# Optimization experiments

Measured on AMD Instinct MI355X. Metric: run time of the kernel, lower is better.

The kernel has to match this reference:

```python
import jax, jax.numpy as jnp
import numpy as np

PATCH = 16
EPS = 1e-5


def _conv_offsets(x, offset_w, offset_b):
    # offset conv: same kernel/stride/padding as the deform conv
    off = jax.lax.conv_general_dilated(
        x, offset_w, window_strides=(PATCH, PATCH), padding='VALID',
        dimension_numbers=('NCHW', 'OIHW', 'NCHW'))
    return off + offset_b[None, :, None, None]


def _deform_conv(x, offset_w, offset_b, dconv_w):
    B, C, H, W = x.shape
    kh = kw = PATCH
    K = kh * kw
    Ho, Wo = H // PATCH, W // PATCH

    off = _conv_offsets(x, offset_w, offset_b)            # [B, 2K, Ho, Wo]
    # mmcv layout: channels are (dy, dx) pairs per kernel point
    off = off.reshape(B, K, 2, Ho, Wo)
    dy = off[:, :, 0].transpose(0, 2, 3, 1)               # [B, Ho, Wo, K]
    dx = off[:, :, 1].transpose(0, 2, 3, 1)

    ii, jj = jnp.meshgrid(jnp.arange(kh), jnp.arange(kw), indexing='ij')
    ki = ii.reshape(-1).astype(x.dtype)                   # [K]
    kj = jj.reshape(-1).astype(x.dtype)
    base_y = (jnp.arange(Ho, dtype=x.dtype) * PATCH)[:, None] + ki[None, :]  # [Ho, K]
    base_x = (jnp.arange(Wo, dtype=x.dtype) * PATCH)[:, None] + kj[None, :]  # [Wo, K]

    py = base_y[None, :, None, :] + dy                    # [B, Ho, Wo, K]
    px = base_x[None, None, :, :] + dx

    y0 = jnp.floor(py); x0 = jnp.floor(px)
    wy1 = py - y0; wx1 = px - x0
    wy0 = 1.0 - wy1; wx0 = 1.0 - wx1
    y0i = y0.astype(jnp.int32); x0i = x0.astype(jnp.int32)
    y1i = y0i + 1;              x1i = x0i + 1

    xt = x.transpose(0, 2, 3, 1)                          # [B, H, W, C]
    bidx = jnp.arange(B)[:, None, None, None]

    def gather(yi, xi):
        ok = ((yi >= 0) & (yi < H) & (xi >= 0) & (xi < W)).astype(x.dtype)
        v = xt[bidx, jnp.clip(yi, 0, H - 1), jnp.clip(xi, 0, W - 1)]  # [B,Ho,Wo,K,C]
        return v * ok[..., None]

    sampled = (gather(y0i, x0i) * (wy0 * wx0)[..., None]
               + gather(y0i, x1i) * (wy0 * wx1)[..., None]
               + gather(y1i, x0i) * (wy1 * wx0)[..., None]
               + gather(y1i, x1i) * (wy1 * wx1)[..., None])  # [B,Ho,Wo,K,C]

    Wk = dconv_w.reshape(dconv_w.shape[0], C, K)          # [O, C, K]
    out = jnp.einsum('bhwkc,ock->bohw', sampled, Wk)      # [B, O, Ho, Wo]
    return out


def setup_inputs() -> dict:
    key = jax.random.key(0)
    ks = jax.random.split(key, 3)
    B, C, H, W = 64, 3, 224, 224
    O = 768
    x = jax.random.normal(ks[0], (B, C, H, W), jnp.float32)
    # small offset weights -> offsets of O(1) pixel, exercising bilinear path
    offset_w = jax.random.normal(ks[1], (2 * PATCH * PATCH, C, PATCH, PATCH), jnp.float32) * 0.01
    offset_b = jnp.zeros((2 * PATCH * PATCH,), jnp.float32)
    dconv_w = jax.random.normal(ks[2], (O, C, PATCH, PATCH), jnp.float32) * 0.02
    bn_gamma = jnp.ones((O,), jnp.float32)
    bn_beta = jnp.zeros((O,), jnp.float32)
    return {"x": x, "offset_w": offset_w, "offset_b": offset_b,
            "dconv_w": dconv_w, "bn_gamma": bn_gamma, "bn_beta": bn_beta}


def reference(x, offset_w, offset_b, dconv_w, bn_gamma, bn_beta):
    B = x.shape[0]
    y = _deform_conv(x, offset_w, offset_b, dconv_w)      # [B, O, Ho, Wo]
    # BatchNorm2d (training-mode batch stats, biased var) per torch semantics
    mean = jnp.mean(y, axis=(0, 2, 3), keepdims=True)
    var = jnp.mean((y - mean) ** 2, axis=(0, 2, 3), keepdims=True)
    yn = (y - mean) * jax.lax.rsqrt(var + EPS)
    yn = yn * bn_gamma[None, :, None, None] + bn_beta[None, :, None, None]
    ya = jax.nn.gelu(yn, approximate=False)               # nn.GELU default = exact
    O, Ho, Wo = ya.shape[1], ya.shape[2], ya.shape[3]
    return ya.reshape(B, O, Ho * Wo).transpose(0, 2, 1)   # [B, N, embed_dim]
```

## Files before the change

### kernel.cpp

```cpp
#include <hip/hip_runtime.h>
#include <math.h>

#define PATCH 16
#define BATCH 64
#define CIN 3
#define HH 224
#define WW 224
#define NPATCH (BATCH*14*14)
#define KDIM 768
#define NOFF 512
#define NOUT 768
#define KPTS 256
#define EPSF 1e-5f
#define CHW (CIN*HH*WW)
#define HWX (HH*WW)
#define NRB (NPATCH/128)

using short8 = __attribute__((ext_vector_type(8))) short;
using f32x4  = __attribute__((ext_vector_type(4))) float;

#define GLOAD16(g, l) __builtin_amdgcn_global_load_lds( \
    (const __attribute__((address_space(1))) void*)(g), \
    (__attribute__((address_space(3))) void*)(l), 16, 0, 0)

__device__ __forceinline__ unsigned short f2bf(float f) {
    unsigned int u = __float_as_uint(f);
    u = (u + 0x7fffu + ((u >> 16) & 1u)) >> 16;
    return (unsigned short)u;
}
__device__ __forceinline__ float bf2f(unsigned short h) {
    return __uint_as_float(((unsigned int)h) << 16);
}
__device__ __forceinline__ float gelu_exact(float v) {
    return 0.5f * v * (1.0f + erff(v * 0.70710678118654752440f));
}

#define N4X (BATCH*CHW/4)
#define N4W1 (NOFF*KDIM/4)
#define N4W2 (NOUT*KDIM/4)
#define N4ALL (N4X+N4W1+N4W2)

__global__ __launch_bounds__(256) void cvt_all(
    const float* __restrict__ x, const float* __restrict__ w1,
    const float* __restrict__ w2, unsigned short* __restrict__ xbf,
    unsigned short* __restrict__ wbf1, unsigned short* __restrict__ wbf2)
{
    for (int i = blockIdx.x*256 + threadIdx.x; i < N4ALL; i += gridDim.x*256) {
        const float* src; unsigned short* dst; int j;
        if (i < N4X)            { src = x;  dst = xbf;  j = i; }
        else if (i < N4X+N4W1)  { src = w1; dst = wbf1; j = i - N4X; }
        else                    { src = w2; dst = wbf2; j = i - N4X - N4W1; }
        float4 v = ((const float4*)src)[j];
        ((ushort4*)dst)[j] = make_ushort4(f2bf(v.x), f2bf(v.y), f2bf(v.z), f2bf(v.w));
    }
}

__global__ __launch_bounds__(256) void gemm_offsets(
    const unsigned short* __restrict__ xbf, const unsigned short* __restrict__ Bw,
    const float* __restrict__ offb, unsigned short* __restrict__ off)
{
    __shared__ unsigned short lds[4*8192];
    const int t = threadIdx.x;
    const int lane = t & 63;
    const int w = t >> 6, wr = w >> 1, wc = w & 1;

    int bid = blockIdx.x;
    int idx = (bid & 7)*49 + (bid >> 3);
    const int bm = (idx >> 2) * 128, bn = (idx & 3) * 128;

    const int rq = t >> 2;
    const int ksw = (((t & 3) ^ ((t >> 3) & 3)) << 3);

    const unsigned short* aBase0;
    const unsigned short* aBase1;
    {
        int p0 = bm + rq,      b0 = p0/196, r0 = p0%196;
        int p1 = bm + 64 + rq, b1 = p1/196, r1 = p1%196;
        aBase0 = xbf + (size_t)b0*CHW + (size_t)((r0/14)*PATCH)*WW + (size_t)((r0%14)*PATCH);
        aBase1 = xbf + (size_t)b1*CHW + (size_t)((r1/14)*PATCH)*WW + (size_t)((r1%14)*PATCH);
    }
    const unsigned short* bS0 = Bw + (size_t)(bn + rq)*KDIM + ksw;
    const unsigned short* bS1 = Bw + (size_t)(bn + 64 + rq)*KDIM + ksw;

    const int row_a = wr*64 + (lane & 15);
    const int row_b = wc*64 + (lane & 15);
    const int klocs = (((lane >> 4) ^ ((lane >> 1) & 3)) << 3);

#define STG1(slot, k0) do { \
        unsigned short* d = lds + (slot)*8192 + t*8; \
        int e = (k0) + ksw; \
        size_t xo = (size_t)(e >> 8)*HWX + (size_t)((e >> 4) & 15)*WW + (e & 15); \
        GLOAD16(aBase0 + xo, d); \
        GLOAD16(aBase1 + xo, d + 2048); \
        GLOAD16(bS0 + (k0), d + 4096); \
        GLOAD16(bS1 + (k0), d + 6144); \
    } while(0)

    f32x4 acc[4][4] = {};
    STG1(0, 0); STG1(1, 32); STG1(2, 64);
    asm volatile("s_waitcnt vmcnt(8)" ::: "memory");
    __builtin_amdgcn_s_barrier();
#pragma unroll
    for (int it = 0; it < 24; ++it) {
        if (it + 3 < 24) STG1((it+3)&3, (it+3)*32);
        const unsigned short* As_ = lds + (it&3)*8192;
        const unsigned short* Bs_ = As_ + 4096;
        short8 af[4], bv[4];
#pragma unroll
        for (int m = 0; m < 4; ++m) af[m] = *(const short8*)&As_[(row_a + m*16)*32 + klocs];
#pragma unroll
        for (int n = 0; n < 4; ++n) bv[n] = *(const short8*)&Bs_[(row_b + n*16)*32 + klocs];
        __builtin_amdgcn_s_setprio(1);
#pragma unroll
        for (int m = 0; m < 4; ++m)
#pragma unroll
            for (int n = 0; n < 4; ++n)
                acc[m][n] = __builtin_amdgcn_mfma_f32_16x16x32_bf16(af[m], bv[n], acc[m][n], 0, 0, 0);
        __builtin_amdgcn_s_setprio(0);
        if (it <= 20)      { asm volatile("s_waitcnt vmcnt(8) lgkmcnt(0)" ::: "memory"); __builtin_amdgcn_s_barrier(); }
        else if (it == 21) { asm volatile("s_waitcnt vmcnt(4) lgkmcnt(0)" ::: "memory"); __builtin_amdgcn_s_barrier(); }
        else if (it == 22) { asm volatile("s_waitcnt vmcnt(0) lgkmcnt(0)" ::: "memory"); __builtin_amdgcn_s_barrier(); }
    }
#undef STG1

    const int col0 = bn + wc*64 + (lane & 15);
    const int r0 = (lane >> 4) * 4;
#pragma unroll
    for (int m = 0; m < 4; ++m) {
        int grow = bm + wr*64 + m*16 + r0;
#pragma unroll
        for (int n = 0; n < 4; ++n) {
            int gcol = col0 + n*16;
            float bias = offb[gcol];
#pragma unroll
            for (int r = 0; r < 4; ++r)
                off[(size_t)(grow + r)*NOFF + gcol] = f2bf(acc[m][n][r] + bias);
        }
    }
}

__global__ __launch_bounds__(256) void sampler(
    const unsigned short* __restrict__ xbf, const unsigned int* __restrict__ offu,
    unsigned short* __restrict__ A2)
{
    __shared__ unsigned short win[3][22][24];
    int p = blockIdx.x;
    int k = threadIdx.x;
    int b = p / 196, rem = p % 196;
    int ho = rem / 14, wo = rem % 14;
    const int gy0 = ho*PATCH - 2, gx0 = wo*PATCH - 2;
    const unsigned short* xb = xbf + (size_t)b*CHW;

    bool interior = (ho >= 1) && (ho <= 12) && (wo >= 1) && (wo <= 12);
    if (interior) {
        for (int idx = k; idx < 3*22*11; idx += 256) {
            int c = idx / 242, r2 = idx - c*242;
            int row = r2 / 11, u = r2 - row*11;
            const unsigned int* src = (const unsigned int*)
                (xb + (size_t)c*HWX + (size_t)(gy0+row)*WW + gx0);
            *(unsigned int*)&win[c][row][2*u] = src[u];
        }
    } else {
        for (int idx = k; idx < 3*22*22; idx += 256) {
            int c = idx / 484, r2 = idx - c*484;
            int row = r2 / 22, col = r2 - row*22;
            int gy = min(max(gy0+row, 0), HH-1);
            int gx = min(max(gx0+col, 0), WW-1);
            win[c][row][col] = xb[(size_t)c*HWX + (size_t)gy*WW + gx];
        }
    }
    __syncthreads();

    unsigned int d2 = offu[(size_t)p*KPTS + k];
    float dy = __uint_as_float((d2 & 0xffffu) << 16);
    float dx = __uint_as_float(d2 & 0xffff0000u);
    float py = (float)(ho*PATCH + (k >> 4)) + dy;
    float px = (float)(wo*PATCH + (k & 15)) + dx;
    float fy = floorf(py), fx = floorf(px);
    float wy1 = py - fy, wx1 = px - fx;
    float wy0 = 1.f - wy1, wx0 = 1.f - wx1;
    int y0 = (int)fy, x0 = (int)fx;
    int y1 = y0 + 1, x1 = x0 + 1;
    bool oky0 = (y0 >= 0) & (y0 < HH);
    bool oky1 = (y1 >= 0) & (y1 < HH);
    bool okx0 = (x0 >= 0) & (x0 < WW);
    bool okx1 = (x1 >= 0) & (x1 < WW);
    float w00 = wy0*wx0, w01 = wy0*wx1, w10 = wy1*wx0, w11 = wy1*wx1;

    int ry = y0 - gy0, rx = x0 - gx0;
    if (ry >= 0 && ry <= 20 && rx >= 0 && rx <= 20) {
        float m00 = oky0 && okx0 ? 1.f : 0.f;
        float m01 = oky0 && okx1 ? 1.f : 0.f;
        float m10 = oky1 && okx0 ? 1.f : 0.f;
        float m11 = oky1 && okx1 ? 1.f : 0.f;
#pragma unroll
        for (int c = 0; c < CIN; ++c) {
            float v00 = bf2f(win[c][ry  ][rx  ]) * m00;
            float v01 = bf2f(win[c][ry  ][rx+1]) * m01;
            float v10 = bf2f(win[c][ry+1][rx  ]) * m10;
            float v11 = bf2f(win[c][ry+1][rx+1]) * m11;
            float v = v00*w00 + v01*w01 + v10*w10 + v11*w11;
            A2[(size_t)p*KDIM + c*KPTS + k] = f2bf(v);
        }
    } else {
        int yc0 = min(max(y0, 0), HH-1), yc1 = min(max(y1, 0), HH-1);
        int xc0 = min(max(x0, 0), WW-1), xc1 = min(max(x1, 0), WW-1);
#pragma unroll
        for (int c = 0; c < CIN; ++c) {
            const unsigned short* xc = xb + (size_t)c*HWX;
            float v00 = (oky0 && okx0) ? bf2f(xc[(size_t)yc0*WW + xc0]) : 0.f;
            float v01 = (oky0 && okx1) ? bf2f(xc[(size_t)yc0*WW + xc1]) : 0.f;
            float v10 = (oky1 && okx0) ? bf2f(xc[(size_t)yc1*WW + xc0]) : 0.f;
            float v11 = (oky1 && okx1) ? bf2f(xc[(size_t)yc1*WW + xc1]) : 0.f;
            float v = v00*w00 + v01*w01 + v10*w10 + v11*w11;
            A2[(size_t)p*KDIM + c*KPTS + k] = f2bf(v);
        }
    }
}

__global__ __launch_bounds__(512) void gemm_deform(
    const unsigned short* __restrict__ A, const unsigned short* __restrict__ Bw,
    unsigned short* __restrict__ Cbf, float* __restrict__ psum, float* __restrict__ psq)
{
    __shared__ unsigned short lds[4*16384];
    const int t = threadIdx.x;
    const int lane = t & 63;
    const int w = t >> 6;
    const int wr = w >> 2, wc = w & 3;

    int bid = blockIdx.x;
    int xcd = bid & 7, jj = bid >> 3;
    int idx = (xcd < 3) ? xcd*19 + jj : 57 + (xcd-3)*18 + jj;
    const int mblk = idx / 3;
    const int bm = mblk*256, bn = (idx % 3)*256;

    const int schunk = ((t & 3) ^ ((t >> 3) & 3)) << 3;
    const unsigned short* aSrc = A  + (size_t)(bm + (t >> 2))*KDIM + schunk;
    const unsigned short* bSrc = Bw + (size_t)(bn + (t >> 2))*KDIM + schunk;

#define STG_A(s, k0) do { \
        unsigned short* d = lds + (s)*16384 + t*8; \
        GLOAD16(aSrc + (k0), d); \
        GLOAD16(aSrc + (size_t)128*KDIM + (k0), d + 4096); } while(0)
#define STG_B(s, k0) do { \
        unsigned short* d = lds + (s)*16384 + 8192 + t*8; \
        GLOAD16(bSrc + (k0), d); \
        GLOAD16(bSrc + (size_t)128*KDIM + (k0), d + 4096); } while(0)

    const int klocs = (((lane >> 4) ^ ((lane >> 1) & 3)) << 3);
    const int arow0 = wr*128 + (lane & 15);
    const int brow0 = wc*64  + (lane & 15);

    f32x4 acc[8][4] = {};

    STG_A(0, 0);  STG_B(0, 0);
    STG_A(1, 32); STG_B(1, 32);
    asm volatile("s_waitcnt vmcnt(4)" ::: "memory");
    __builtin_amdgcn_s_barrier();

    short8 af[8], bv[4];
    for (int kt = 0; kt < 12; ++kt) {
        const int s0 = (2*kt) & 3;
        const int s1 = s0 + 1;
        const int s2 = (s0 + 2) & 3;
        const int s3 = (s0 + 3) & 3;
        const int k2 = (2*kt + 2) * 32;
        const int k3 = (2*kt + 3) * 32;
        const unsigned short* H0 = lds + s0*16384;
        const unsigned short* H1 = lds + s1*16384;

#pragma unroll
        for (int m = 0; m < 8; ++m) af[m] = *(const short8*)&H0[(arow0 + m*16)*32 + klocs];
        bv[0] = *(const short8*)&H0[8192 + (brow0 +  0)*32 + klocs];
        bv[1] = *(const short8*)&H0[8192 + (brow0 + 16)*32 + klocs];
        if (kt < 11) STG_A(s2, k2);
        __builtin_amdgcn_s_barrier();
        asm volatile("s_waitcnt lgkmcnt(0)" ::: "memory");
        __builtin_amdgcn_s_setprio(1);
#pragma unroll
        for (int m = 0; m < 8; ++m) {
            acc[m][0] = __builtin_amdgcn_mfma_f32_16x16x32_bf16(af[m], bv[0], acc[m][0], 0, 0, 0);
            acc[m][1] = __builtin_amdgcn_mfma_f32_16x16x32_bf16(af[m], bv[1], acc[m][1], 0, 0, 0);
        }
        __builtin_amdgcn_s_setprio(0);

        bv[2] = *(const short8*)&H0[8192 + (brow0 + 32)*32 + klocs];
        bv[3] = *(const short8*)&H0[8192 + (brow0 + 48)*32 + klocs];
        if (kt < 11) { STG_B(s2, k2);
            asm volatile("s_waitcnt vmcnt(4)" ::: "memory");
        } else {
            asm volatile("s_waitcnt vmcnt(0)" ::: "memory");
        }
        __builtin_amdgcn_s_barrier();
        asm volatile("s_waitcnt lgkmcnt(0)" ::: "memory");
        __builtin_amdgcn_s_setprio(1);
#pragma unroll
        for (int m = 0; m < 8; ++m) {
            acc[m][2] = __builtin_amdgcn_mfma_f32_16x16x32_bf16(af[m], bv[2], acc[m][2], 0, 0, 0);
            acc[m][3] = __builtin_amdgcn_mfma_f32_16x16x32_bf16(af[m], bv[3], acc[m][3], 0, 0, 0);
        }
        __builtin_amdgcn_s_setprio(0);

#pragma unroll
        for (int m = 0; m < 8; ++m) af[m] = *(const short8*)&H1[(arow0 + m*16)*32 + klocs];
        bv[0] = *(const short8*)&H1[8192 + (brow0 +  0)*32 + klocs];
        bv[1] = *(const short8*)&H1[8192 + (brow0 + 16)*32 + klocs];
        if (kt < 11) STG_A(s3, k3);
        __builtin_amdgcn_s_barrier();
        asm volatile("s_waitcnt lgkmcnt(0)" ::: "memory");
        __builtin_amdgcn_s_setprio(1);
#pragma unroll
        for (int m = 0; m < 8; ++m) {
            acc[m][0] = __builtin_amdgcn_mfma_f32_16x16x32_bf16(af[m], bv[0], acc[m][0], 0, 0, 0);
            acc[m][1] = __builtin_amdgcn_mfma_f32_16x16x32_bf16(af[m], bv[1], acc[m][1], 0, 0, 0);
        }
        __builtin_amdgcn_s_setprio(0);

        bv[2] = *(const short8*)&H1[8192 + (brow0 + 32)*32 + klocs];
        bv[3] = *(const short8*)&H1[8192 + (brow0 + 48)*32 + klocs];
        if (kt < 11) { STG_B(s3, k3);
            asm volatile("s_waitcnt vmcnt(4)" ::: "memory");
        }
        __builtin_amdgcn_s_barrier();
        asm volatile("s_waitcnt lgkmcnt(0)" ::: "memory");
        __builtin_amdgcn_s_setprio(1);
#pragma unroll
        for (int m = 0; m < 8; ++m) {
            acc[m][2] = __builtin_amdgcn_mfma_f32_16x16x32_bf16(af[m], bv[2], acc[m][2], 0, 0, 0);
            acc[m][3] = __builtin_amdgcn_mfma_f32_16x16x32_bf16(af[m], bv[3], acc[m][3], 0, 0, 0);
        }
        __builtin_amdgcn_s_setprio(0);
    }
#undef STG_A
#undef STG_B

    asm volatile("s_waitcnt lgkmcnt(0)" ::: "memory");

    float s[4] = {}, q[4] = {};
#pragma unroll
    for (int m = 0; m < 8; ++m)
#pragma unroll
        for (int n = 0; n < 4; ++n)
#pragma unroll
            for (int r = 0; r < 4; ++r) {
                float v = acc[m][n][r];
                s[n] += v; q[n] += v*v;
            }
#pragma unroll
    for (int n = 0; n < 4; ++n) {
        s[n] += __shfl_xor(s[n], 16); q[n] += __shfl_xor(q[n], 16);
        s[n] += __shfl_xor(s[n], 32); q[n] += __shfl_xor(q[n], 32);
    }

    __syncthreads();
    float* redS = (float*)lds;
    float* redQ = redS + 512;
    if (lane < 16) {
#pragma unroll
        for (int n = 0; n < 4; ++n) {
            redS[wr*256 + wc*64 + n*16 + lane] = s[n];
            redQ[wr*256 + wc*64 + n*16 + lane] = q[n];
        }
    }
    __syncthreads();

    const int col0 = bn + wc*64 + (lane & 15);
    const int r0 = (lane >> 4) * 4;
#pragma unroll
    for (int m = 0; m < 8; ++m) {
        int grow = bm + wr*128 + m*16 + r0;
#pragma unroll
        for (int n = 0; n < 4; ++n) {
            int gcol = col0 + n*16;
#pragma unroll
            for (int r = 0; r < 4; ++r)
                Cbf[(size_t)(grow + r)*NOUT + gcol] = f2bf(acc[m][n][r]);
        }
    }
    {
        int half = t >> 8;
        int c = t & 255;
        psum[(size_t)(bm/128 + half)*NOUT + bn + c] = redS[half*256 + c];
        psq [(size_t)(bm/128 + half)*NOUT + bn + c] = redQ[half*256 + c];
    }
}

__global__ __launch_bounds__(256) void bn_final(
    const float* __restrict__ psum, const float* __restrict__ psq,
    const float* __restrict__ gamma, const float* __restrict__ beta,
    float* __restrict__ scale, float* __restrict__ shift)
{
    int o = blockIdx.x*256 + threadIdx.x;
    float s = 0.f, q = 0.f;
    for (int i = 0; i < NRB; ++i) {
        s += psum[(size_t)i*NOUT + o];
        q += psq [(size_t)i*NOUT + o];
    }
    float mean = s * (1.0f/(float)NPATCH);
    float var  = q * (1.0f/(float)NPATCH) - mean*mean;
    float inv  = 1.0f / sqrtf(var + EPSF);
    float sc   = gamma[o] * inv;
    scale[o] = sc;
    shift[o] = beta[o] - mean*sc;
}

__global__ __launch_bounds__(256) void norm_gelu(
    const unsigned short* __restrict__ ybf, float* __restrict__ out,
    const float* __restrict__ scale, const float* __restrict__ shift)
{
    __shared__ float ssc[NOUT], ssh[NOUT];
    for (int i = threadIdx.x; i < NOUT; i += 256) { ssc[i] = scale[i]; ssh[i] = shift[i]; }
    __syncthreads();
    const size_t total8 = (size_t)NPATCH * NOUT / 8;
    for (size_t i = (size_t)blockIdx.x*256 + threadIdx.x; i < total8;
         i += (size_t)gridDim.x*256) {
        uint4 v = ((const uint4*)ybf)[i];
        int og = (int)(i % (NOUT/8)) * 8;
        float4 o0, o1;
        o0.x = gelu_exact(__uint_as_float(v.x << 16)        * ssc[og+0] + ssh[og+0]);
        o0.y = gelu_exact(__uint_as_float(v.x & 0xffff0000u)* ssc[og+1] + ssh[og+1]);
        o0.z = gelu_exact(__uint_as_float(v.y << 16)        * ssc[og+2] + ssh[og+2]);
        o0.w = gelu_exact(__uint_as_float(v.y & 0xffff0000u)* ssc[og+3] + ssh[og+3]);
        o1.x = gelu_exact(__uint_as_float(v.z << 16)        * ssc[og+4] + ssh[og+4]);
        o1.y = gelu_exact(__uint_as_float(v.z & 0xffff0000u)* ssc[og+5] + ssh[og+5]);
        o1.z = gelu_exact(__uint_as_float(v.w << 16)        * ssc[og+6] + ssh[og+6]);
        o1.w = gelu_exact(__uint_as_float(v.w & 0xffff0000u)* ssc[og+7] + ssh[og+7]);
        ((float4*)out)[2*i]   = o0;
        ((float4*)out)[2*i+1] = o1;
    }
}

extern "C" void kernel_launch(void* const* d_in, const int* in_sizes, int n_in,
                              void* d_out, int out_size, void* d_ws, size_t ws_size,
                              hipStream_t stream)
{
    const float* x      = (const float*)d_in[0];
    const float* offw   = (const float*)d_in[1];
    const float* offb   = (const float*)d_in[2];
    const float* dconvw = (const float*)d_in[3];
    const float* gamma  = (const float*)d_in[4];
    const float* beta   = (const float*)d_in[5];
    float* out = (float*)d_out;

    const size_t NX  = (size_t)BATCH*CHW;
    const size_t NW1 = (size_t)NOFF*KDIM;
    const size_t NW2 = (size_t)NOUT*KDIM;

    unsigned short* xbf   = (unsigned short*)d_ws;
    unsigned short* wbf1  = xbf  + NX;
    unsigned short* wbf2  = wbf1 + NW1;
    unsigned short* A2    = wbf2 + NW2;
    unsigned short* off   = A2   + (size_t)NPATCH*KDIM;
    unsigned short* ybf   = off  + (size_t)NPATCH*NOFF;
    float* fscratch = (float*)(ybf + (size_t)NPATCH*NOUT);
    float* psum  = fscratch;
    float* psq   = psum + NRB*NOUT;
    float* scale = psq  + NRB*NOUT;
    float* shift = scale + NOUT;

    cvt_all<<<4096, 256, 0, stream>>>(x, offw, dconvw, xbf, wbf1, wbf2);
    gemm_offsets<<<392, 256, 0, stream>>>(xbf, wbf1, offb, off);
    sampler<<<NPATCH, 256, 0, stream>>>(xbf, (const unsigned int*)off, A2);
    gemm_deform<<<147, 512, 0, stream>>>(A2, wbf2, ybf, psum, psq);
    bn_final<<<3, 256, 0, stream>>>(psum, psq, gamma, beta, scale, shift);
    norm_gelu<<<2048, 256, 0, stream>>>(ybf, out, scale, shift);
}
```

Baseline: 100.3 us.

## Fuse batchnorm stats and GELU into deform GEMM via cooperative grid sync

The deform GEMM now runs as a cooperative kernel. After writing per-block partial sums it performs a grid-wide sync, then each block computes BN scale/shift for its 256 columns and applies them plus exact GELU directly to the accumulators before writing fp32 output. This removes the bf16 intermediate write/read round trip and two extra kernel launches. The cost is a grid barrier while holding a large accumulator register file, and a requirement that all 147 blocks be co-resident.

Result: slower. 164.1 us (+63.6%).

```diff
diff --git a/kernel.cpp b/kernel.cpp
--- a/kernel.cpp
+++ b/kernel.cpp
@@ -1,4 +1,5 @@
 #include <hip/hip_runtime.h>
+#include <hip/hip_cooperative_groups.h>
 #include <math.h>
 
 #define PATCH 16
@@ -220,7 +221,8 @@
 
 __global__ __launch_bounds__(512) void gemm_deform(
     const unsigned short* __restrict__ A, const unsigned short* __restrict__ Bw,
-    unsigned short* __restrict__ Cbf, float* __restrict__ psum, float* __restrict__ psq)
+    float* __restrict__ out, float* __restrict__ psum, float* __restrict__ psq,
+    const float* __restrict__ gamma, const float* __restrict__ beta)
 {
     __shared__ unsigned short lds[4*16384];
     const int t = threadIdx.x;
@@ -363,70 +365,46 @@
         }
     }
     __syncthreads();
-
-    const int col0 = bn + wc*64 + (lane & 15);
-    const int r0 = (lane >> 4) * 4;
-#pragma unroll
-    for (int m = 0; m < 8; ++m) {
-        int grow = bm + wr*128 + m*16 + r0;
-#pragma unroll
-        for (int n = 0; n < 4; ++n) {
-            int gcol = col0 + n*16;
-#pragma unroll
-            for (int r = 0; r < 4; ++r)
-                Cbf[(size_t)(grow + r)*NOUT + gcol] = f2bf(acc[m][n][r]);
-        }
-    }
     {
         int half = t >> 8;
         int c = t & 255;
         psum[(size_t)(bm/128 + half)*NOUT + bn + c] = redS[half*256 + c];
         psq [(size_t)(bm/128 + half)*NOUT + bn + c] = redQ[half*256 + c];
     }
-}
-
-__global__ __launch_bounds__(256) void bn_final(
-    const float* __restrict__ psum, const float* __restrict__ psq,
-    const float* __restrict__ gamma, const float* __restrict__ beta,
-    float* __restrict__ scale, float* __restrict__ shift)
-{
-    int o = blockIdx.x*256 + threadIdx.x;
-    float s = 0.f, q = 0.f;
-    for (int i = 0; i < NRB; ++i) {
-        s += psum[(size_t)i*NOUT + o];
-        q += psq [(size_t)i*NOUT + o];
-    }
-    float mean = s * (1.0f/(float)NPATCH);
-    float var  = q * (1.0f/(float)NPATCH) - mean*mean;
-    float inv  = 1.0f / sqrtf(var + EPSF);
-    float sc   = gamma[o] * inv;
-    scale[o] = sc;
-    shift[o] = beta[o] - mean*sc;
-}
-
-__global__ __launch_bounds__(256) void norm_gelu(
-    const unsigned short* __restrict__ ybf, float* __restrict__ out,
-    const float* __restrict__ scale, const float* __restrict__ shift)
-{
-    __shared__ float ssc[NOUT], ssh[NOUT];
-    for (int i = threadIdx.x; i < NOUT; i += 256) { ssc[i] = scale[i]; ssh[i] = shift[i]; }
+
+    __threadfence();
+    cooperative_groups::this_grid().sync();
+
+    float* ssc = (float*)lds;
+    float* ssh = ssc + 256;
+    if (t < 256) {
+        float s2 = 0.f, q2 = 0.f;
+        for (int i = 0; i < NRB; ++i) {
+            s2 += psum[(size_t)i*NOUT + bn + t];
+            q2 += psq [(size_t)i*NOUT + bn + t];
+        }
+        float mean = s2 * (1.0f/(float)NPATCH);
+        float var  = q2 * (1.0f/(float)NPATCH) - mean*mean;
+        float inv  = 1.0f / sqrtf(var + EPSF);
+        float sc   = gamma[bn + t] * inv;
+        ssc[t] = sc;
+        ssh[t] = beta[bn + t] - mean*sc;
+    }
     __syncthreads();
-    const size_t total8 = (size_t)NPATCH * NOUT / 8;
-    for (size_t i = (size_t)blockIdx.x*256 + threadIdx.x; i < total8;
-         i += (size_t)gridDim.x*256) {
-        uint4 v = ((const uint4*)ybf)[i];
-        int og = (int)(i % (NOUT/8)) * 8;
-        float4 o0, o1;
-        o0.x = gelu_exact(__uint_as_float(v.x << 16)        * ssc[og+0] + ssh[og+0]);
-        o0.y = gelu_exact(__uint_as_float(v.x & 0xffff0000u)* ssc[og+1] + ssh[og+1]);
-        o0.z = gelu_exact(__uint_as_float(v.y << 16)        * ssc[og+2] + ssh[og+2]);
-        o0.w = gelu_exact(__uint_as_float(v.y & 0xffff0000u)* ssc[og+3] + ssh[og+3]);
-        o1.x = gelu_exact(__uint_as_float(v.z << 16)        * ssc[og+4] + ssh[og+4]);
-        o1.y = gelu_exact(__uint_as_float(v.z & 0xffff0000u)* ssc[og+5] + ssh[og+5]);
-        o1.z = gelu_exact(__uint_as_float(v.w << 16)        * ssc[og+6] + ssh[og+6]);
-        o1.w = gelu_exact(__uint_as_float(v.w & 0xffff0000u)* ssc[og+7] + ssh[og+7]);
-        ((float4*)out)[2*i]   = o0;
-        ((float4*)out)[2*i+1] = o1;
+
+    const int col0l = wc*64 + (lane & 15);
+    const int r0 = (lane >> 4) * 4;
+#pragma unroll
+    for (int m = 0; m < 8; ++m) {
+        int grow = bm + wr*128 + m*16 + r0;
+#pragma unroll
+        for (int n = 0; n < 4; ++n) {
+            int cl = col0l + n*16;
+            float sc = ssc[cl], sh = ssh[cl];
+#pragma unroll
+            for (int r = 0; r < 4; ++r)
+                out[(size_t)(grow + r)*NOUT + bn + cl] = gelu_exact(acc[m][n][r]*sc + sh);
+        }
     }
 }
 
@@ -451,17 +429,20 @@
     unsigned short* wbf2  = wbf1 + NW1;
     unsigned short* A2    = wbf2 + NW2;
     unsigned short* off   = A2   + (size_t)NPATCH*KDIM;
-    unsigned short* ybf   = off  + (size_t)NPATCH*NOFF;
-    float* fscratch = (float*)(ybf + (size_t)NPATCH*NOUT);
+    float* fscratch = (float*)(off + (size_t)NPATCH*NOFF);
     float* psum  = fscratch;
     float* psq   = psum + NRB*NOUT;
-    float* scale = psq  + NRB*NOUT;
-    float* shift = scale + NOUT;
 
     cvt_all<<<4096, 256, 0, stream>>>(x, offw, dconvw, xbf, wbf1, wbf2);
     gemm_offsets<<<392, 256, 0, stream>>>(xbf, wbf1, offb, off);
     sampler<<<NPATCH, 256, 0, stream>>>(xbf, (const unsigned int*)off, A2);
-    gemm_deform<<<147, 512, 0, stream>>>(A2, wbf2, ybf, psum, psq);
-    bn_final<<<3, 256, 0, stream>>>(psum, psq, gamma, beta, scale, shift);
-    norm_gelu<<<2048, 256, 0, stream>>>(ybf, out, scale, shift);
-}
+
+    {
+        const unsigned short* A2c = A2;
+        const unsigned short* Wc  = wbf2;
+        void* args[] = { (void*)&A2c, (void*)&Wc, (void*)&out,
+                         (void*)&psum, (void*)&psq, (void*)&gamma, (void*)&beta };
+        hipLaunchCooperativeKernel((const void*)gemm_deform, dim3(147), dim3(512),
+                                   args, 0, stream);
+    }
+}
```
